# Kernel tuning notes

Hardware: AMD Instinct MI355X
Metric: run time of the kernel (lower is better)

## Reference

```python
import jax, jax.numpy as jnp
import numpy as np

N = 50000   # nodes
E = 300000  # directed edges (~Delaunay mesh, degree 6)
H = 128     # hidden_size
TW = 5      # time_window
P = 3       # process_steps
NODE_IN = 9
EDGE_IN = 4
LN_EPS = 1e-5


def _ln(x, g, b):
    m = jnp.mean(x, axis=-1, keepdims=True)
    v = jnp.var(x, axis=-1, keepdims=True)
    return (x - m) * jax.lax.rsqrt(v + LN_EPS) * g + b


def _mlp_ln(x, w1, b1, w2, b2, g, bb):
    # Linear -> ReLU -> Linear -> LayerNorm (matches MLP(..., layer_norm=True))
    h = jax.nn.relu(x @ w1 + b1)
    return _ln(h @ w2 + b2, g, bb)


def setup_inputs() -> dict:
    key = jax.random.key(0)
    ks = iter(jax.random.split(key, 64))
    def nrm(shape):
        return jax.random.normal(next(ks), shape, jnp.float32)
    def lin(fi, fo, stack=None):
        sh = (fi, fo) if stack is None else (stack, fi, fo)
        return nrm(sh) / np.sqrt(fi)
    inp = {}
    inp["temperature"] = nrm((N,))
    inp["temperature_prev"] = nrm((N,))
    inp["heat_source"] = nrm((N,))
    inp["heat_source_prev"] = nrm((N,))
    inp["heat_source_next"] = nrm((N, TW))
    inp["mesh_pos"] = jax.random.uniform(next(ks), (N, 2), jnp.float32)
    inp["edge_index"] = jax.random.randint(next(ks), (2, E), 0, N, jnp.int32)
    # Normalizer params (running mean/std)
    inp["node_norm_mean"] = jnp.zeros((NODE_IN,), jnp.float32)
    inp["node_norm_std"] = jnp.ones((NODE_IN,), jnp.float32)
    inp["edge_norm_mean"] = jnp.zeros((EDGE_IN,), jnp.float32)
    inp["edge_norm_std"] = jnp.ones((EDGE_IN,), jnp.float32)
    # node encoder
    inp["ne_w1"] = lin(NODE_IN, H); inp["ne_b1"] = jnp.zeros((H,), jnp.float32)
    inp["ne_w2"] = lin(H, H);       inp["ne_b2"] = jnp.zeros((H,), jnp.float32)
    inp["ne_g"] = jnp.ones((H,), jnp.float32); inp["ne_be"] = jnp.zeros((H,), jnp.float32)
    # edge encoder
    inp["ee_w1"] = lin(EDGE_IN, H); inp["ee_b1"] = jnp.zeros((H,), jnp.float32)
    inp["ee_w2"] = lin(H, H);       inp["ee_b2"] = jnp.zeros((H,), jnp.float32)
    inp["ee_g"] = jnp.ones((H,), jnp.float32); inp["ee_be"] = jnp.zeros((H,), jnp.float32)
    # processors (stacked over P steps): edge_mlp in=3H, node_mlp in=2H
    inp["pe_w1"] = lin(3 * H, H, P); inp["pe_b1"] = jnp.zeros((P, H), jnp.float32)
    inp["pe_w2"] = lin(H, H, P);     inp["pe_b2"] = jnp.zeros((P, H), jnp.float32)
    inp["pe_g"] = jnp.ones((P, H), jnp.float32); inp["pe_be"] = jnp.zeros((P, H), jnp.float32)
    inp["pn_w1"] = lin(2 * H, H, P); inp["pn_b1"] = jnp.zeros((P, H), jnp.float32)
    inp["pn_w2"] = lin(H, H, P);     inp["pn_b2"] = jnp.zeros((P, H), jnp.float32)
    inp["pn_g"] = jnp.ones((P, H), jnp.float32); inp["pn_be"] = jnp.zeros((P, H), jnp.float32)
    # decoder (Conv1d kernel_size=1 == per-node Linear), Swish in between
    inp["dec_w1"] = lin(H, H // 2); inp["dec_b1"] = jnp.zeros((H // 2,), jnp.float32)
    inp["dec_w2"] = lin(H // 2, TW); inp["dec_b2"] = jnp.zeros((TW,), jnp.float32)
    return inp


def reference(temperature, temperature_prev, heat_source, heat_source_prev,
              heat_source_next, mesh_pos, edge_index,
              node_norm_mean, node_norm_std, edge_norm_mean, edge_norm_std,
              ne_w1, ne_b1, ne_w2, ne_b2, ne_g, ne_be,
              ee_w1, ee_b1, ee_w2, ee_b2, ee_g, ee_be,
              pe_w1, pe_b1, pe_w2, pe_b2, pe_g, pe_be,
              pn_w1, pn_b1, pn_w2, pn_b2, pn_g, pn_be,
              dec_w1, dec_b1, dec_w2, dec_b2):
    u = temperature
    # node features: [u, u_dot, q, q_dot, q_next]  -> [N, 9]
    x = jnp.concatenate([
        u[:, None], (u - temperature_prev)[:, None],
        heat_source[:, None], (heat_source - heat_source_prev)[:, None],
        heat_source_next], axis=-1)
    s, r = edge_index[0], edge_index[1]  # senders (source j), receivers (target i)
    rel = mesh_pos[s] - mesh_pos[r]                       # [E, 2]
    dist = jnp.linalg.norm(rel, axis=-1, keepdims=True)   # [E, 1]
    relt = (u[s] - u[r])[:, None]                         # [E, 1]
    e = jnp.concatenate([rel, dist, relt], axis=-1)       # [E, 4]

    xh = _mlp_ln((x - node_norm_mean) / node_norm_std, ne_w1, ne_b1, ne_w2, ne_b2, ne_g, ne_be)
    eh = _mlp_ln((e - edge_norm_mean) / edge_norm_std, ee_w1, ee_b1, ee_w2, ee_b2, ee_g, ee_be)

    n_nodes = xh.shape[0]
    for i in range(P):
        xs, xr = xh[s], xh[r]  # x_j = x[source], x_i = x[target]
        # message: edge_mlp(cat[x_i, x_j, e]) then scatter-add at target index
        msg = _mlp_ln(jnp.concatenate([xr, xs, eh], axis=-1),
                      pe_w1[i], pe_b1[i], pe_w2[i], pe_b2[i], pe_g[i], pe_be[i])
        aggr = jax.ops.segment_sum(msg, r, num_segments=n_nodes)
        # node update + residual
        new_x = _mlp_ln(jnp.concatenate([aggr, xh], axis=-1),
                        pn_w1[i], pn_b1[i], pn_w2[i], pn_b2[i], pn_g[i], pn_be[i]) + xh
        # edge update (note row/col ordering differs from message) + residual
        new_e = _mlp_ln(jnp.concatenate([xs, xr, eh], axis=-1),
                        pe_w1[i], pe_b1[i], pe_w2[i], pe_b2[i], pe_g[i], pe_be[i]) + eh
        xh, eh = new_x, new_e

    # decoder: 1x1 convs == per-node linears, Swish(beta=1) activation
    h = xh @ dec_w1 + dec_b1
    h = h * jax.nn.sigmoid(h)
    delta = (h @ dec_w2 + dec_b2).reshape(-1, TW)
    dt = jnp.arange(1, TW + 1, dtype=delta.dtype)
    return dt[None, :] * delta
```

## Files before the change

kernel.cpp:

```cpp
#include <hip/hip_runtime.h>
#include <stdint.h>

typedef unsigned short u16;
typedef __attribute__((ext_vector_type(8))) short bf16x8_t;
typedef __attribute__((ext_vector_type(4))) float f32x4_t;

__device__ __forceinline__ float bl(u16 x) {
  union { unsigned u; float f; } c; c.u = ((unsigned)x) << 16; return c.f;
}
__device__ __forceinline__ u16 fb(float x) {
  union { float f; unsigned u; } c; c.f = x;
  unsigned r = c.u + 0x7fffu + ((c.u >> 16) & 1u);
  return (u16)(r >> 16);
}

__global__ void sentinel_kernel(float* out, int n) {
  int i = blockIdx.x * 256 + threadIdx.x;
  if (i < n) out[i] = 12345.f;
}

struct TSeg { const float* src; u16* dst; };
struct TArgs { TSeg s[23]; };
__global__ void transpose_w(TArgs a) {
  const float* src = a.s[blockIdx.x].src;
  u16* dst = a.s[blockIdx.x].dst;
  for (int e = threadIdx.x; e < 16384; e += 256) {
    int n = e >> 7, k = e & 127;
    dst[e] = fb(src[k * 128 + n]);
  }
}

__global__ void zero_i32(int* p, int n) {
  int i = blockIdx.x * 256 + threadIdx.x;
  if (i < n) p[i] = 0;
}
__global__ void deg_count(const int* __restrict__ ei, int* __restrict__ cnt, int E) {
  int e = blockIdx.x * 256 + threadIdx.x;
  if (e < E) atomicAdd(&cnt[ei[E + e]], 1);
}
__global__ void scan1(const int* __restrict__ cnt, int* __restrict__ part,
                      int* __restrict__ bsum, int N) {
  __shared__ int s[256];
  int i = blockIdx.x * 256 + threadIdx.x;
  s[threadIdx.x] = (i < N) ? cnt[i] : 0;
  __syncthreads();
#pragma unroll
  for (int o = 1; o < 256; o <<= 1) {
    int t = (threadIdx.x >= o) ? s[threadIdx.x - o] : 0;
    __syncthreads();
    s[threadIdx.x] += t;
    __syncthreads();
  }
  if (i < N) part[i] = s[threadIdx.x];
  if (threadIdx.x == 255) bsum[blockIdx.x] = s[255];
}
__global__ void scan2(int* bsum, int nb) {
  if (threadIdx.x == 0 && blockIdx.x == 0) {
    int acc = 0;
    for (int i = 0; i < nb; ++i) { int t = bsum[i]; bsum[i] = acc; acc += t; }
  }
}
__global__ void scan3(const int* __restrict__ part, const int* __restrict__ bsum,
                      int* __restrict__ start, int N) {
  int i = blockIdx.x * 256 + threadIdx.x;
  if (i < N) start[i + 1] = part[i] + bsum[i >> 8];
  if (i == 0) start[0] = 0;
}
__global__ void fill_slot(const int* __restrict__ ei, int* __restrict__ cnt2,
                          const int* __restrict__ start, int* __restrict__ sortedS,
                          int* __restrict__ sortedR, int E) {
  int e = blockIdx.x * 256 + threadIdx.x;
  if (e >= E) return;
  int s = ei[e], r = ei[E + e];
  int p = atomicAdd(&cnt2[r], 1);
  int slot = start[r] + p;
  sortedS[slot] = s;
  sortedR[slot] = r;
}

__global__ void aggregate(const u16* __restrict__ msgbuf, const int* __restrict__ start,
                          u16* __restrict__ aggrb, int N) {
  int n = blockIdx.x * 16 + (threadIdx.x >> 4);
  int t = threadIdx.x & 15;
  if (n >= N) return;
  int b = start[n], e = start[n + 1];
  float acc[8] = {0, 0, 0, 0, 0, 0, 0, 0};
  for (int i = b; i < e; ++i) {
    u16 m8[8];
    *(uint4*)m8 = *(const uint4*)(msgbuf + (size_t)i * 128 + t * 8);
#pragma unroll
    for (int j = 0; j < 8; ++j) acc[j] += bl(m8[j]);
  }
  u16 o8[8];
#pragma unroll
  for (int j = 0; j < 8; ++j) o8[j] = fb(acc[j]);
  *(uint4*)(aggrb + (size_t)n * 128 + t * 8) = *(uint4*)o8;
}

__global__ void node_feat_kernel(const float* __restrict__ t, const float* __restrict__ tp,
                                 const float* __restrict__ q, const float* __restrict__ qp,
                                 const float* __restrict__ qn, const float* __restrict__ nm,
                                 const float* __restrict__ ns, float* __restrict__ nfeat,
                                 int n_nodes) {
  int n = blockIdx.x * 256 + threadIdx.x;
  if (n >= n_nodes) return;
  float u = t[n];
  float x[9];
  x[0] = u; x[1] = u - tp[n];
  float hq = q[n];
  x[2] = hq; x[3] = hq - qp[n];
#pragma unroll
  for (int j = 0; j < 5; ++j) x[4 + j] = qn[n * 5 + j];
#pragma unroll
  for (int k = 0; k < 9; ++k) nfeat[n * 9 + k] = (x[k] - nm[k]) / ns[k];
}

__global__ void edge_feat_kernel(const int* __restrict__ sArr, const int* __restrict__ rArr,
                                 const float* __restrict__ mp, const float* __restrict__ u,
                                 const float* __restrict__ em, const float* __restrict__ es,
                                 float* __restrict__ efeat, int n_edges) {
  int e = blockIdx.x * 256 + threadIdx.x;
  if (e >= n_edges) return;
  int s = sArr[e], r = rArr[e];
  float rx = mp[s * 2] - mp[r * 2];
  float ry = mp[s * 2 + 1] - mp[r * 2 + 1];
  float d = sqrtf(rx * rx + ry * ry);
  float rt = u[s] - u[r];
  float x[4] = {rx, ry, d, rt};
#pragma unroll
  for (int k = 0; k < 4; ++k) efeat[e * 4 + k] = (x[k] - em[k]) / es[k];
}

template <int K>
__global__ void enc1_kernel(const float* __restrict__ feat, const float* __restrict__ w1,
                            const float* __restrict__ b1, u16* __restrict__ out, int M) {
  int gid = blockIdx.x * 256 + threadIdx.x;
  int n = gid >> 7, h = gid & 127;
  if (n >= M) return;
  float acc = b1[h];
#pragma unroll
  for (int k = 0; k < K; ++k) acc += feat[n * K + k] * w1[k * 128 + h];
  out[n * 128 + h] = fb(acc > 0.f ? acc : 0.f);
}

#define GM_NONE 0
#define GM_RELU 1
#define GM_LN 2

template <int MODE, bool DUAL, bool A0F32>
__global__ __launch_bounds__(256, 2) void gemm64(
    const void* __restrict__ A0v, const u16* __restrict__ WT0, const u16* __restrict__ A1,
    const u16* __restrict__ WT1, const float* __restrict__ bias, const float* __restrict__ gg,
    const float* __restrict__ bb, const u16* __restrict__ resid, u16* __restrict__ out, int M) {
  __shared__ u16 sO[64][136];
  const int tid = threadIdx.x;
  const int wave = tid >> 6, lane = tid & 63;
  const int q = lane >> 4, l16 = lane & 15;
  const int m0 = blockIdx.x * 64;
  int arow = m0 + wave * 16 + l16;
  if (arow >= M) arow = M - 1;

  f32x4_t acc[8];
#pragma unroll
  for (int b = 0; b < 8; ++b) acc[b] = (f32x4_t){0.f, 0.f, 0.f, 0.f};

  const int NKT = DUAL ? 2 : 1;
#pragma unroll 1
  for (int kt = 0; kt < NKT; ++kt) {
    const u16* WT = kt ? WT1 : WT0;
#pragma unroll
    for (int kk = 0; kk < 4; ++kk) {
      bf16x8_t af;
      if (A0F32 && kt == 0) {
        const float* ap = (const float*)A0v + (size_t)arow * 128 + kk * 32 + q * 8;
        union { u16 u[8]; bf16x8_t v; } cv;
#pragma unroll
        for (int j = 0; j < 8; ++j) cv.u[j] = fb(ap[j]);
        af = cv.v;
      } else {
        const u16* ap = (kt ? A1 : (const u16*)A0v) + (size_t)arow * 128 + kk * 32 + q * 8;
        af = *(const bf16x8_t*)ap;
      }
      const u16* wp = WT + kk * 32 + q * 8;
#pragma unroll
      for (int nt = 0; nt < 8; ++nt) {
        bf16x8_t bfv = *(const bf16x8_t*)(wp + (size_t)(nt * 16 + l16) * 128);
        acc[nt] = __builtin_amdgcn_mfma_f32_16x16x32_bf16(af, bfv, acc[nt], 0, 0, 0);
      }
    }
  }

  const int rowb = wave * 16 + q * 4;
  if (MODE == GM_NONE) {
#pragma unroll
    for (int r = 0; r < 4; ++r)
#pragma unroll
      for (int nt = 0; nt < 8; ++nt) sO[rowb + r][nt * 16 + l16] = fb(acc[nt][r]);
  } else if (MODE == GM_RELU) {
    float bcol[8];
#pragma unroll
    for (int nt = 0; nt < 8; ++nt) bcol[nt] = bias[nt * 16 + l16];
#pragma unroll
    for (int r = 0; r < 4; ++r)
#pragma unroll
      for (int nt = 0; nt < 8; ++nt) {
        float v = acc[nt][r] + bcol[nt];
        sO[rowb + r][nt * 16 + l16] = fb(v > 0.f ? v : 0.f);
      }
  } else {
    float bcol[8], gcol[8], becol[8];
#pragma unroll
    for (int nt = 0; nt < 8; ++nt) {
      bcol[nt] = bias[nt * 16 + l16];
      gcol[nt] = gg[nt * 16 + l16];
      becol[nt] = bb[nt * 16 + l16];
    }
    float s[4] = {0, 0, 0, 0}, ss[4] = {0, 0, 0, 0};
#pragma unroll
    for (int r = 0; r < 4; ++r)
#pragma unroll
      for (int nt = 0; nt < 8; ++nt) {
        float v = acc[nt][r] + bcol[nt];
        s[r] += v;
        ss[r] += v * v;
      }
#pragma unroll
    for (int r = 0; r < 4; ++r) {
#pragma unroll
      for (int m = 1; m <= 8; m <<= 1) {
        s[r] += __shfl_xor(s[r], m, 64);
        ss[r] += __shfl_xor(ss[r], m, 64);
      }
    }
#pragma unroll
    for (int r = 0; r < 4; ++r) {
      float mean = s[r] * (1.f / 128.f);
      float var = fmaxf(ss[r] * (1.f / 128.f) - mean * mean, 0.f);
      float rstd = rsqrtf(var + 1e-5f);
#pragma unroll
      for (int nt = 0; nt < 8; ++nt) {
        float v = (acc[nt][r] + bcol[nt] - mean) * rstd * gcol[nt] + becol[nt];
        sO[rowb + r][nt * 16 + l16] = fb(v);
      }
    }
  }
  __syncthreads();
#pragma unroll
  for (int it = 0; it < 4; ++it) {
    int lin = it * 256 + tid;
    int row = lin >> 4, ch = (lin & 15) * 8;
    int grow = m0 + row;
    if (grow >= M) continue;
    u16 o8[8];
    *(uint4*)o8 = *(uint4*)(&sO[row][ch]);
    if (MODE == GM_LN && resid) {
      u16 r8[8];
      *(uint4*)r8 = *(const uint4*)(resid + (size_t)grow * 128 + ch);
#pragma unroll
      for (int j = 0; j < 8; ++j) o8[j] = fb(bl(o8[j]) + bl(r8[j]));
    }
    *(uint4*)(out + (size_t)grow * 128 + ch) = *(uint4*)o8;
  }
}

__global__ __launch_bounds__(256, 2) void gemm64_2w(
    const u16* __restrict__ A, const u16* __restrict__ WT0, const u16* __restrict__ WT1,
    u16* __restrict__ out0, u16* __restrict__ out1, int M) {
  __shared__ u16 sO0[64][136];
  __shared__ u16 sO1[64][136];
  const int tid = threadIdx.x;
  const int wave = tid >> 6, lane = tid & 63;
  const int q = lane >> 4, l16 = lane & 15;
  const int m0 = blockIdx.x * 64;
  int arow = m0 + wave * 16 + l16;
  if (arow >= M) arow = M - 1;

  f32x4_t a0[8], a1[8];
#pragma unroll
  for (int b = 0; b < 8; ++b) {
    a0[b] = (f32x4_t){0.f, 0.f, 0.f, 0.f};
    a1[b] = (f32x4_t){0.f, 0.f, 0.f, 0.f};
  }
#pragma unroll 2
  for (int kk = 0; kk < 4; ++kk) {
    bf16x8_t af = *(const bf16x8_t*)(A + (size_t)arow * 128 + kk * 32 + q * 8);
#pragma unroll
    for (int nt = 0; nt < 8; ++nt) {
      bf16x8_t b0 = *(const bf16x8_t*)(WT0 + (size_t)(nt * 16 + l16) * 128 + kk * 32 + q * 8);
      bf16x8_t b1v = *(const bf16x8_t*)(WT1 + (size_t)(nt * 16 + l16) * 128 + kk * 32 + q * 8);
      a0[nt] = __builtin_amdgcn_mfma_f32_16x16x32_bf16(af, b0, a0[nt], 0, 0, 0);
      a1[nt] = __builtin_amdgcn_mfma_f32_16x16x32_bf16(af, b1v, a1[nt], 0, 0, 0);
    }
  }
  const int rowb = wave * 16 + q * 4;
#pragma unroll
  for (int r = 0; r < 4; ++r)
#pragma unroll
    for (int nt = 0; nt < 8; ++nt) {
      sO0[rowb + r][nt * 16 + l16] = fb(a0[nt][r]);
      sO1[rowb + r][nt * 16 + l16] = fb(a1[nt][r]);
    }
  __syncthreads();
#pragma unroll
  for (int it = 0; it < 4; ++it) {
    int lin = it * 256 + tid;
    int row = lin >> 4, ch = (lin & 15) * 8;
    int grow = m0 + row;
    if (grow >= M) continue;
    *(uint4*)(out0 + (size_t)grow * 128 + ch) = *(uint4*)(&sO0[row][ch]);
    *(uint4*)(out1 + (size_t)grow * 128 + ch) = *(uint4*)(&sO1[row][ch]);
  }
}

template <bool CSR>
__global__ __launch_bounds__(256, 2) void edge_fused(
    u16* __restrict__ eh, const u16* __restrict__ xhA, const u16* __restrict__ xhB,
    const u16* __restrict__ wtC, const float* __restrict__ b1, const u16* __restrict__ wt2,
    const float* __restrict__ b2, const float* __restrict__ gg, const float* __restrict__ bb,
    const int* __restrict__ sArr, const int* __restrict__ rArr, u16* __restrict__ msgbuf,
    float* __restrict__ scat, int E) {
  __shared__ u16 sHm[64][136];
  __shared__ u16 sHe[64][136];
  __shared__ int sS[64], sR[64];
  const int tid = threadIdx.x;
  const int wave = tid >> 6, lane = tid & 63;
  const int q = lane >> 4, l16 = lane & 15;
  const int m0 = blockIdx.x * 64;
  const int rowb = wave * 16 + q * 4;
  int arow = m0 + wave * 16 + l16;
  int arc = arow < E ? arow : E - 1;

  if (tid < 64) {
    int e = m0 + tid;
    sS[tid] = (e < E) ? sArr[e] : 0;
    sR[tid] = (e < E) ? rArr[e] : 0;
  }

  f32x4_t accC[8];
#pragma unroll
  for (int b = 0; b < 8; ++b) accC[b] = (f32x4_t){0.f, 0.f, 0.f, 0.f};
#pragma unroll
  for (int kk = 0; kk < 4; ++kk) {
    bf16x8_t af = *(const bf16x8_t*)(eh + (size_t)arc * 128 + kk * 32 + q * 8);
#pragma unroll
    for (int nt = 0; nt < 8; ++nt) {
      bf16x8_t bfv = *(const bf16x8_t*)(wtC + (size_t)(nt * 16 + l16) * 128 + kk * 32 + q * 8);
      accC[nt] = __builtin_amdgcn_mfma_f32_16x16x32_bf16(af, bfv, accC[nt], 0, 0, 0);
    }
  }
#pragma unroll
  for (int r = 0; r < 4; ++r)
#pragma unroll
    for (int nt = 0; nt < 8; ++nt) sHm[rowb + r][nt * 16 + l16] = fb(accC[nt][r]);
  __syncthreads();

#pragma unroll
  for (int it = 0; it < 4; ++it) {
    int lin = it * 256 + tid;
    int row = lin >> 4, ch = (lin & 15) * 8;
    bool ok = (m0 + row) < E;
    int s_ = sS[row], r_ = sR[row];
    u16 t8[8], ar[8], as_[8], br[8], bs[8], hm[8], he[8];
    *(uint4*)t8 = *(uint4*)(&sHm[row][ch]);
    *(uint4*)ar = *(const uint4*)(xhA + (size_t)r_ * 128 + ch);
    *(uint4*)as_ = *(const uint4*)(xhA + (size_t)s_ * 128 + ch);
    *(uint4*)br = *(const uint4*)(xhB + (size_t)r_ * 128 + ch);
    *(uint4*)bs = *(const uint4*)(xhB + (size_t)s_ * 128 + ch);
#pragma unroll
    for (int j = 0; j < 8; ++j) {
      float t = bl(t8[j]) + b1[ch + j];
      float vm = t + bl(ar[j]) + bl(bs[j]);
      float ve = t + bl(as_[j]) + bl(br[j]);
      hm[j] = (ok && vm > 0.f) ? fb(vm) : 0;
      he[j] = (ok && ve > 0.f) ? fb(ve) : 0;
    }
    *(uint4*)(&sHm[row][ch]) = *(uint4*)hm;
    *(uint4*)(&sHe[row][ch]) = *(uint4*)he;
  }
  __syncthreads();

  float bcol[8], gcol[8], becol[8];
#pragma unroll
  for (int nt = 0; nt < 8; ++nt) {
    bcol[nt] = b2[nt * 16 + l16];
    gcol[nt] = gg[nt * 16 + l16];
    becol[nt] = bb[nt * 16 + l16];
  }

  f32x4_t accM[8], accE[8];
#pragma unroll
  for (int b = 0; b < 8; ++b) {
    accM[b] = (f32x4_t){0.f, 0.f, 0.f, 0.f};
    accE[b] = (f32x4_t){0.f, 0.f, 0.f, 0.f};
  }
#pragma unroll
  for (int kk = 0; kk < 4; ++kk) {
    bf16x8_t afm = *(const bf16x8_t*)(&sHm[wave * 16 + l16][kk * 32 + q * 8]);
    bf16x8_t afe = *(const bf16x8_t*)(&sHe[wave * 16 + l16][kk * 32 + q * 8]);
#pragma unroll
    for (int nt = 0; nt < 8; ++nt) {
      bf16x8_t bfv = *(const bf16x8_t*)(wt2 + (size_t)(nt * 16 + l16) * 128 + kk * 32 + q * 8);
      accM[nt] = __builtin_amdgcn_mfma_f32_16x16x32_bf16(afm, bfv, accM[nt], 0, 0, 0);
      accE[nt] = __builtin_amdgcn_mfma_f32_16x16x32_bf16(afe, bfv, accE[nt], 0, 0, 0);
    }
  }
  float sm[4] = {0, 0, 0, 0}, ssm[4] = {0, 0, 0, 0};
  float se[4] = {0, 0, 0, 0}, sse[4] = {0, 0, 0, 0};
#pragma unroll
  for (int r = 0; r < 4; ++r)
#pragma unroll
    for (int nt = 0; nt < 8; ++nt) {
      float vm = accM[nt][r] + bcol[nt];
      float ve = accE[nt][r] + bcol[nt];
      sm[r] += vm; ssm[r] += vm * vm;
      se[r] += ve; sse[r] += ve * ve;
    }
#pragma unroll
  for (int r = 0; r < 4; ++r) {
#pragma unroll
    for (int m = 1; m <= 8; m <<= 1) {
      sm[r] += __shfl_xor(sm[r], m, 64);
      ssm[r] += __shfl_xor(ssm[r], m, 64);
      se[r] += __shfl_xor(se[r], m, 64);
      sse[r] += __shfl_xor(sse[r], m, 64);
    }
  }

  if (!CSR) {
#pragma unroll
    for (int r = 0; r < 4; ++r) {
      int row = m0 + rowb + r;
      if (row >= E) continue;
      int rr = sR[rowb + r];
      float mean = sm[r] * (1.f / 128.f);
      float var = fmaxf(ssm[r] * (1.f / 128.f) - mean * mean, 0.f);
      float rstd = rsqrtf(var + 1e-5f);
#pragma unroll
      for (int nt = 0; nt < 8; ++nt) {
        float v = (accM[nt][r] + bcol[nt] - mean) * rstd * gcol[nt] + becol[nt];
        atomicAdd(&scat[(size_t)rr * 128 + nt * 16 + l16], v);
      }
    }
  }

  __syncthreads();
#pragma unroll
  for (int r = 0; r < 4; ++r) {
    float meanE = se[r] * (1.f / 128.f);
    float varE = fmaxf(sse[r] * (1.f / 128.f) - meanE * meanE, 0.f);
    float rstdE = rsqrtf(varE + 1e-5f);
    float meanM = sm[r] * (1.f / 128.f);
    float varM = fmaxf(ssm[r] * (1.f / 128.f) - meanM * meanM, 0.f);
    float rstdM = rsqrtf(varM + 1e-5f);
#pragma unroll
    for (int nt = 0; nt < 8; ++nt) {
      float ve = (accE[nt][r] + bcol[nt] - meanE) * rstdE * gcol[nt] + becol[nt];
      sHe[rowb + r][nt * 16 + l16] = fb(ve);
      if (CSR) {
        float vm = (accM[nt][r] + bcol[nt] - meanM) * rstdM * gcol[nt] + becol[nt];
        sHm[rowb + r][nt * 16 + l16] = fb(vm);
      }
    }
  }
  __syncthreads();
#pragma unroll
  for (int it = 0; it < 4; ++it) {
    int lin = it * 256 + tid;
    int row = lin >> 4, ch = (lin & 15) * 8;
    int grow = m0 + row;
    if (grow >= E) continue;
    if (CSR) {
      *(uint4*)(msgbuf + (size_t)grow * 128 + ch) = *(uint4*)(&sHm[row][ch]);
    }
    u16 y8[8], e8[8];
    *(uint4*)y8 = *(uint4*)(&sHe[row][ch]);
    *(uint4*)e8 = *(const uint4*)(eh + (size_t)grow * 128 + ch);
#pragma unroll
    for (int j = 0; j < 8; ++j) y8[j] = fb(bl(y8[j]) + bl(e8[j]));
    *(uint4*)(eh + (size_t)grow * 128 + ch) = *(uint4*)y8;
  }
}

__global__ void decoder_kernel(const u16* __restrict__ xh, const float* __restrict__ w1,
                               const float* __restrict__ b1, const float* __restrict__ w2,
                               const float* __restrict__ b2, float* __restrict__ out,
                               int n_nodes) {
  __shared__ float sx[4][128];
  int tid = threadIdx.x;
  int lw = tid >> 6, lane = tid & 63;
  int n0 = blockIdx.x * 4;
  for (int i = tid; i < 512; i += 256) {
    int nn = i >> 7, c = i & 127;
    int n = n0 + nn;
    sx[nn][c] = (n < n_nodes) ? bl(xh[(size_t)n * 128 + c]) : 0.f;
  }
  __syncthreads();
  int n = n0 + lw;
  float h = b1[lane];
#pragma unroll 16
  for (int k = 0; k < 128; ++k) h += sx[lw][k] * w1[k * 64 + lane];
  float hs = h * (1.f / (1.f + __expf(-h)));
  float d[5];
#pragma unroll
  for (int t = 0; t < 5; ++t) {
    float p = hs * w2[lane * 5 + t];
#pragma unroll
    for (int m = 1; m <= 32; m <<= 1) p += __shfl_xor(p, m, 64);
    d[t] = p;
  }
  if (lane == 0 && n < n_nodes) {
#pragma unroll
    for (int t = 0; t < 5; ++t)
      out[(size_t)n * 5 + t] = (float)(t + 1) * (d[t] + b2[t]);
  }
}

extern "C" void kernel_launch(void* const* d_in, const int* in_sizes, int n_in, void* d_out,
                              int out_size, void* d_ws, size_t ws_size, hipStream_t stream) {
  auto F = [&](int i) { return (const float*)d_in[i]; };
  const int* edge_index = (const int*)d_in[6];
  const int N_ = in_sizes[0];
  const int E_ = in_sizes[6] / 2;

  char* wsb = (char*)d_ws;
  size_t off = 0;
  auto alloc = [&](size_t bytes) -> char* {
    char* p = wsb + off;
    off += (bytes + 255) & ~(size_t)255;
    return p;
  };
  u16* xh = (u16*)alloc((size_t)N_ * 128 * 2);
  u16* xhA = (u16*)alloc((size_t)N_ * 128 * 2);
  u16* xhB = (u16*)alloc((size_t)N_ * 128 * 2);
  u16* h1n = (u16*)alloc((size_t)N_ * 128 * 2);
  u16* ehP = (u16*)alloc((size_t)E_ * 128 * 2);
  float* nfeat = (float*)xhA;
  float* efeat = (float*)xhB;
  u16* aggrb = xhA;
  u16* wne2T = (u16*)alloc(16384 * 2);
  u16* wee2T = (u16*)alloc(16384 * 2);
  u16* wpe1T = (u16*)alloc((size_t)9 * 16384 * 2);
  u16* wpe2T = (u16*)alloc((size_t)3 * 16384 * 2);
  u16* wpn1T = (u16*)alloc((size_t)6 * 16384 * 2);
  u16* wpn2T = (u16*)alloc((size_t)3 * 16384 * 2);

  const size_t base_off = off;
  int* startp = (int*)alloc((size_t)(N_ + 1) * 4);
  int* cntp = (int*)alloc((size_t)N_ * 4);
  int* partp = (int*)alloc((size_t)N_ * 4);
  int* bsump = (int*)alloc(((size_t)(N_ + 255) / 256) * 4 + 256);
  int* sortedS = (int*)alloc((size_t)E_ * 4);
  int* sortedR = (int*)alloc((size_t)E_ * 4);
  u16* msgbuf = (u16*)alloc((size_t)E_ * 128 * 2);
  bool useCSR = (off <= ws_size);
  float* aggrf = nullptr;
  if (!useCSR) {
    off = base_off;
    aggrf = (float*)alloc((size_t)N_ * 128 * 4);
    if (off > ws_size) {
      sentinel_kernel<<<(out_size + 255) / 256, 256, 0, stream>>>((float*)d_out, out_size);
      return;
    }
  }

  TArgs ta;
  int ts = 0;
  ta.s[ts++] = {F(13), wne2T};
  ta.s[ts++] = {F(19), wee2T};
  for (int i = 0; i < 3; ++i)
    for (int b = 0; b < 3; ++b)
      ta.s[ts++] = {F(23) + (size_t)(i * 3 + b) * 16384, wpe1T + (size_t)(i * 3 + b) * 16384};
  for (int i = 0; i < 3; ++i) ta.s[ts++] = {F(25) + (size_t)i * 16384, wpe2T + (size_t)i * 16384};
  for (int i = 0; i < 3; ++i)
    for (int b = 0; b < 2; ++b)
      ta.s[ts++] = {F(29) + (size_t)(i * 2 + b) * 16384, wpn1T + (size_t)(i * 2 + b) * 16384};
  for (int i = 0; i < 3; ++i) ta.s[ts++] = {F(31) + (size_t)i * 16384, wpn2T + (size_t)i * 16384};

  const int tilesN = (N_ + 63) / 64;
  const int tilesE = (E_ + 63) / 64;
  const int nb = (N_ + 255) / 256;
  dim3 blk(256);

  transpose_w<<<23, blk, 0, stream>>>(ta);

  const int* sArr = edge_index;
  const int* rArr = edge_index + E_;
  if (useCSR) {
    zero_i32<<<(N_ + 255) / 256, blk, 0, stream>>>(cntp, N_);
    deg_count<<<(E_ + 255) / 256, blk, 0, stream>>>(edge_index, cntp, E_);
    scan1<<<nb, blk, 0, stream>>>(cntp, partp, bsump, N_);
    scan2<<<1, blk, 0, stream>>>(bsump, nb);
    scan3<<<nb, blk, 0, stream>>>(partp, bsump, startp, N_);
    zero_i32<<<(N_ + 255) / 256, blk, 0, stream>>>(cntp, N_);
    fill_slot<<<(E_ + 255) / 256, blk, 0, stream>>>(edge_index, cntp, startp, sortedS, sortedR,
                                                    E_);
    sArr = sortedS;
    rArr = sortedR;
  }

  node_feat_kernel<<<(N_ + 255) / 256, blk, 0, stream>>>(F(0), F(1), F(2), F(3), F(4), F(7),
                                                         F(8), nfeat, N_);
  enc1_kernel<9><<<(N_ * 128 + 255) / 256, blk, 0, stream>>>(nfeat, F(11), F(12), h1n, N_);
  gemm64<GM_LN, false, false><<<tilesN, blk, 0, stream>>>(h1n, wne2T, nullptr, nullptr, F(14),
                                                          F(15), F(16), nullptr, xh, N_);
  edge_feat_kernel<<<(E_ + 255) / 256, blk, 0, stream>>>(sArr, rArr, F(5), F(0), F(9), F(10),
                                                         efeat, E_);
  enc1_kernel<4><<<(E_ * 128 + 255) / 256, blk, 0, stream>>>(efeat, F(17), F(18), ehP, E_);
  gemm64<GM_LN, false, false><<<tilesE, blk, 0, stream>>>(ehP, wee2T, nullptr, nullptr, F(20),
                                                          F(21), F(22), nullptr, ehP, E_);

  for (int i = 0; i < 3; ++i) {
    const u16* wtA = wpe1T + (size_t)(i * 3 + 0) * 16384;
    const u16* wtB = wpe1T + (size_t)(i * 3 + 1) * 16384;
    const u16* wtC = wpe1T + (size_t)(i * 3 + 2) * 16384;
    const float* pb1 = F(24) + i * 128;
    const u16* wt2 = wpe2T + (size_t)i * 16384;
    const float* pb2 = F(26) + i * 128;
    const float* pg = F(27) + i * 128;
    const float* pbe = F(28) + i * 128;
    const u16* wtnA = wpn1T + (size_t)(i * 2 + 0) * 16384;
    const u16* wtnB = wpn1T + (size_t)(i * 2 + 1) * 16384;
    const float* nb1 = F(30) + i * 128;
    const u16* wtn2 = wpn2T + (size_t)i * 16384;
    const float* nb2 = F(32) + i * 128;
    const float* ng = F(33) + i * 128;
    const float* nbe = F(34) + i * 128;

    gemm64_2w<<<tilesN, blk, 0, stream>>>(xh, wtA, wtB, xhA, xhB, N_);
    if (useCSR) {
      edge_fused<true><<<tilesE, blk, 0, stream>>>(ehP, xhA, xhB, wtC, pb1, wt2, pb2, pg, pbe,
                                                   sArr, rArr, msgbuf, nullptr, E_);
      aggregate<<<(N_ + 15) / 16, blk, 0, stream>>>(msgbuf, startp, aggrb, N_);
      gemm64<GM_RELU, true, false><<<tilesN, blk, 0, stream>>>(aggrb, wtnA, xh, wtnB, nb1,
                                                               nullptr, nullptr, nullptr, h1n,
                                                               N_);
    } else {
      (void)hipMemsetAsync(aggrf, 0, (size_t)N_ * 128 * 4, stream);
      edge_fused<false><<<tilesE, blk, 0, stream>>>(ehP, xhA, xhB, wtC, pb1, wt2, pb2, pg, pbe,
                                                    sArr, rArr, nullptr, aggrf, E_);
      gemm64<GM_RELU, true, true><<<tilesN, blk, 0, stream>>>(aggrf, wtnA, xh, wtnB, nb1,
                                                              nullptr, nullptr, nullptr, h1n,
                                                              N_);
    }
    gemm64<GM_LN, false, false><<<tilesN, blk, 0, stream>>>(h1n, wtn2, nullptr, nullptr, nb2,
                                                            ng, nbe, xh, xh, N_);
  }

  decoder_kernel<<<(N_ + 3) / 4, blk, 0, stream>>>(xh, F(35), F(36), F(37), F(38),
                                                   (float*)d_out, N_);
}
```

Measured before the change: 1.376 ms.

## Fuse CSR segment aggregation into edge kernel and prefetch source gathers

Removes the separate aggregate kernel and the E×128 bf16 message buffer. Because edges are sorted by receiver, each edge tile now reduces its messages per receiver segment in shared memory. A segment that lies wholly inside the tile is written directly to an fp32 aggregate, and a segment that crosses tiles is added with atomics. Source-node gathers of xhA/xhB are also issued early, before the first MFMA, so their latency overlaps the matmul. This costs a per-step memset of the fp32 aggregate and extra registers for the prefetched data.

```diff
diff --git a/kernel.cpp b/kernel.cpp
--- a/kernel.cpp
+++ b/kernel.cpp
@@ -76,25 +76,6 @@
   int slot = start[r] + p;
   sortedS[slot] = s;
   sortedR[slot] = r;
-}
-
-__global__ void aggregate(const u16* __restrict__ msgbuf, const int* __restrict__ start,
-                          u16* __restrict__ aggrb, int N) {
-  int n = blockIdx.x * 16 + (threadIdx.x >> 4);
-  int t = threadIdx.x & 15;
-  if (n >= N) return;
-  int b = start[n], e = start[n + 1];
-  float acc[8] = {0, 0, 0, 0, 0, 0, 0, 0};
-  for (int i = b; i < e; ++i) {
-    u16 m8[8];
-    *(uint4*)m8 = *(const uint4*)(msgbuf + (size_t)i * 128 + t * 8);
-#pragma unroll
-    for (int j = 0; j < 8; ++j) acc[j] += bl(m8[j]);
-  }
-  u16 o8[8];
-#pragma unroll
-  for (int j = 0; j < 8; ++j) o8[j] = fb(acc[j]);
-  *(uint4*)(aggrb + (size_t)n * 128 + t * 8) = *(uint4*)o8;
 }
 
 __global__ void node_feat_kernel(const float* __restrict__ t, const float* __restrict__ tp,
@@ -317,11 +298,11 @@
     u16* __restrict__ eh, const u16* __restrict__ xhA, const u16* __restrict__ xhB,
     const u16* __restrict__ wtC, const float* __restrict__ b1, const u16* __restrict__ wt2,
     const float* __restrict__ b2, const float* __restrict__ gg, const float* __restrict__ bb,
-    const int* __restrict__ sArr, const int* __restrict__ rArr, u16* __restrict__ msgbuf,
-    float* __restrict__ scat, int E) {
+    const int* __restrict__ sArr, const int* __restrict__ rArr,
+    const int* __restrict__ startp, float* __restrict__ aggr, int E) {
   __shared__ u16 sHm[64][136];
   __shared__ u16 sHe[64][136];
-  __shared__ int sS[64], sR[64];
+  __shared__ int sR[64];
   const int tid = threadIdx.x;
   const int wave = tid >> 6, lane = tid & 63;
   const int q = lane >> 4, l16 = lane & 15;
@@ -332,8 +313,22 @@
 
   if (tid < 64) {
     int e = m0 + tid;
-    sS[tid] = (e < E) ? sArr[e] : 0;
-    sR[tid] = (e < E) ? rArr[e] : 0;
+    sR[tid] = (e < E) ? rArr[e] : -1;
+  }
+
+  int prow[4], pch[4], pr_[4];
+  uint4 pAs[4], pBs[4];
+#pragma unroll
+  for (int it = 0; it < 4; ++it) {
+    int lin = it * 256 + tid;
+    prow[it] = lin >> 4;
+    pch[it] = (lin & 15) * 8;
+    int ge = m0 + prow[it];
+    int gc = ge < E ? ge : E - 1;
+    int ps = sArr[gc];
+    pr_[it] = rArr[gc];
+    pAs[it] = *(const uint4*)(xhA + (size_t)ps * 128 + pch[it]);
+    pBs[it] = *(const uint4*)(xhB + (size_t)ps * 128 + pch[it]);
   }
 
   f32x4_t accC[8];
@@ -356,16 +351,15 @@
 
 #pragma unroll
   for (int it = 0; it < 4; ++it) {
-    int lin = it * 256 + tid;
-    int row = lin >> 4, ch = (lin & 15) * 8;
+    int row = prow[it], ch = pch[it];
     bool ok = (m0 + row) < E;
-    int s_ = sS[row], r_ = sR[row];
+    int r_ = pr_[it] >= 0 ? pr_[it] : 0;
     u16 t8[8], ar[8], as_[8], br[8], bs[8], hm[8], he[8];
     *(uint4*)t8 = *(uint4*)(&sHm[row][ch]);
     *(uint4*)ar = *(const uint4*)(xhA + (size_t)r_ * 128 + ch);
-    *(uint4*)as_ = *(const uint4*)(xhA + (size_t)s_ * 128 + ch);
     *(uint4*)br = *(const uint4*)(xhB + (size_t)r_ * 128 + ch);
-    *(uint4*)bs = *(const uint4*)(xhB + (size_t)s_ * 128 + ch);
+    *(uint4*)as_ = pAs[it];
+    *(uint4*)bs = pBs[it];
 #pragma unroll
     for (int j = 0; j < 8; ++j) {
       float t = bl(t8[j]) + b1[ch + j];
@@ -438,7 +432,7 @@
 #pragma unroll
       for (int nt = 0; nt < 8; ++nt) {
         float v = (accM[nt][r] + bcol[nt] - mean) * rstd * gcol[nt] + becol[nt];
-        atomicAdd(&scat[(size_t)rr * 128 + nt * 16 + l16], v);
+        atomicAdd(&aggr[(size_t)rr * 128 + nt * 16 + l16], v);
       }
     }
   }
@@ -463,21 +457,42 @@
     }
   }
   __syncthreads();
+
 #pragma unroll
   for (int it = 0; it < 4; ++it) {
-    int lin = it * 256 + tid;
-    int row = lin >> 4, ch = (lin & 15) * 8;
+    int row = prow[it], ch = pch[it];
     int grow = m0 + row;
     if (grow >= E) continue;
-    if (CSR) {
-      *(uint4*)(msgbuf + (size_t)grow * 128 + ch) = *(uint4*)(&sHm[row][ch]);
-    }
     u16 y8[8], e8[8];
     *(uint4*)y8 = *(uint4*)(&sHe[row][ch]);
     *(uint4*)e8 = *(const uint4*)(eh + (size_t)grow * 128 + ch);
 #pragma unroll
     for (int j = 0; j < 8; ++j) y8[j] = fb(bl(y8[j]) + bl(e8[j]));
     *(uint4*)(eh + (size_t)grow * 128 + ch) = *(uint4*)y8;
+
+    if (CSR) {
+      int rr = sR[row];
+      bool first = (row == 0) || (sR[row - 1] != rr);
+      if (!first) continue;
+      int gs = startp[rr], ge2 = startp[rr + 1];
+      int le = ge2 - m0;
+      if (le > 64) le = 64;
+      float acc[8] = {0, 0, 0, 0, 0, 0, 0, 0};
+      for (int i = row; i < le; ++i) {
+        u16 m8[8];
+        *(uint4*)m8 = *(uint4*)(&sHm[i][ch]);
+#pragma unroll
+        for (int j = 0; j < 8; ++j) acc[j] += bl(m8[j]);
+      }
+      if (gs >= m0 && ge2 <= m0 + 64) {
+        *(float4*)(aggr + (size_t)rr * 128 + ch) = make_float4(acc[0], acc[1], acc[2], acc[3]);
+        *(float4*)(aggr + (size_t)rr * 128 + ch + 4) =
+            make_float4(acc[4], acc[5], acc[6], acc[7]);
+      } else {
+#pragma unroll
+        for (int j = 0; j < 8; ++j) atomicAdd(&aggr[(size_t)rr * 128 + ch + j], acc[j]);
+      }
+    }
   }
 }
 
@@ -534,9 +549,9 @@
   u16* xhB = (u16*)alloc((size_t)N_ * 128 * 2);
   u16* h1n = (u16*)alloc((size_t)N_ * 128 * 2);
   u16* ehP = (u16*)alloc((size_t)E_ * 128 * 2);
+  float* aggr = (float*)alloc((size_t)N_ * 128 * 4);
   float* nfeat = (float*)xhA;
   float* efeat = (float*)xhB;
-  u16* aggrb = xhA;
   u16* wne2T = (u16*)alloc(16384 * 2);
   u16* wee2T = (u16*)alloc(16384 * 2);
   u16* wpe1T = (u16*)alloc((size_t)9 * 16384 * 2);
@@ -551,12 +566,9 @@
   int* bsump = (int*)alloc(((size_t)(N_ + 255) / 256) * 4 + 256);
   int* sortedS = (int*)alloc((size_t)E_ * 4);
   int* sortedR = (int*)alloc((size_t)E_ * 4);
-  u16* msgbuf = (u16*)alloc((size_t)E_ * 128 * 2);
   bool useCSR = (off <= ws_size);
-  float* aggrf = nullptr;
   if (!useCSR) {
     off = base_off;
-    aggrf = (float*)alloc((size_t)N_ * 128 * 4);
     if (off > ws_size) {
       sentinel_kernel<<<(out_size + 255) / 256, 256, 0, stream>>>((float*)d_out, out_size);
       return;
@@ -627,21 +639,16 @@
     const float* nbe = F(34) + i * 128;
 
     gemm64_2w<<<tilesN, blk, 0, stream>>>(xh, wtA, wtB, xhA, xhB, N_);
+    (void)hipMemsetAsync(aggr, 0, (size_t)N_ * 128 * 4, stream);
     if (useCSR) {
       edge_fused<true><<<tilesE, blk, 0, stream>>>(ehP, xhA, xhB, wtC, pb1, wt2, pb2, pg, pbe,
-                                                   sArr, rArr, msgbuf, nullptr, E_);
-      aggregate<<<(N_ + 15) / 16, blk, 0, stream>>>(msgbuf, startp, aggrb, N_);
-      gemm64<GM_RELU, true, false><<<tilesN, blk, 0, stream>>>(aggrb, wtnA, xh, wtnB, nb1,
-                                                               nullptr, nullptr, nullptr, h1n,
-                                                               N_);
+                                                   sArr, rArr, startp, aggr, E_);
     } else {
-      (void)hipMemsetAsync(aggrf, 0, (size_t)N_ * 128 * 4, stream);
       edge_fused<false><<<tilesE, blk, 0, stream>>>(ehP, xhA, xhB, wtC, pb1, wt2, pb2, pg, pbe,
-                                                    sArr, rArr, nullptr, aggrf, E_);
-      gemm64<GM_RELU, true, true><<<tilesN, blk, 0, stream>>>(aggrf, wtnA, xh, wtnB, nb1,
-                                                              nullptr, nullptr, nullptr, h1n,
-                                                              N_);
-    }
+                                                    sArr, rArr, nullptr, aggr, E_);
+    }
+    gemm64<GM_RELU, true, true><<<tilesN, blk, 0, stream>>>(aggr, wtnA, xh, wtnB, nb1, nullptr,
+                                                            nullptr, nullptr, h1n, N_);
     gemm64<GM_LN, false, false><<<tilesN, blk, 0, stream>>>(h1n, wtn2, nullptr, nullptr, nb2,
                                                             ng, nbe, xh, xh, N_);
   }
```

New measurement: 1.347 ms. 2.1% less time.
